# Kernel tuning notes

Measured on AMD Instinct MI355X. Metric: run time of the kernel, lower is better.

Reference implementation:

```python
import jax, jax.numpy as jnp
import numpy as np

BN_EPS = 1e-5
W_BITS = 2
A_BITS = 2


def _quantize_k(x, k):
    # uniform quantization of x in [0,1] to k bits, straight-through estimator
    n = float(2 ** k - 1)
    q = jnp.round(x * n) / n
    return x + jax.lax.stop_gradient(q - x)


def _quant_weight(w, k):
    # DoReFa-style weight quantization to [-1, 1]
    t = jnp.tanh(w)
    t = t / (2.0 * jnp.max(jnp.abs(t))) + 0.5
    return 2.0 * _quantize_k(t, k) - 1.0


def _quant_act(x, k):
    # DoReFa-style activation quantization: clamp to [0,1], quantize
    return _quantize_k(jnp.clip(x, 0.0, 1.0), k)


def _conv3x3(x, w, stride=1):
    # x: [N,C,H,W], w: [O,I,3,3], padding=1
    return jax.lax.conv_general_dilated(
        x, w, window_strides=(stride, stride), padding=((1, 1), (1, 1)),
        dimension_numbers=('NCHW', 'OIHW', 'NCHW'))


def _bn(x, gamma, beta, mean, var):
    inv = gamma / jnp.sqrt(var + BN_EPS)           # [C]
    return x * inv[None, :, None, None] + (beta - mean * inv)[None, :, None, None]


def setup_inputs() -> dict:
    key = jax.random.key(0)
    ks = jax.random.split(key, 8)
    N, C, H, W = 64, 256, 28, 28
    x = jax.random.normal(ks[0], (N, C, H, W), dtype=jnp.float32)
    w1 = jax.random.normal(ks[1], (C, C, 3, 3), dtype=jnp.float32) * 0.05
    w2 = jax.random.normal(ks[2], (C, C, 3, 3), dtype=jnp.float32) * 0.05
    g1 = jnp.ones((C,), jnp.float32)
    b1 = jnp.zeros((C,), jnp.float32)
    m1 = jax.random.normal(ks[3], (C,), dtype=jnp.float32) * 0.1
    v1 = jax.random.uniform(ks[4], (C,), dtype=jnp.float32) + 0.5
    g2 = jnp.ones((C,), jnp.float32)
    b2 = jnp.zeros((C,), jnp.float32)
    m2 = jax.random.normal(ks[5], (C,), dtype=jnp.float32) * 0.1
    v2 = jax.random.uniform(ks[6], (C,), dtype=jnp.float32) + 0.5
    return {'x': x, 'w1': w1, 'g1': g1, 'b1': b1, 'm1': m1, 'v1': v1,
            'w2': w2, 'g2': g2, 'b2': b2, 'm2': m2, 'v2': v2}


def reference(x, w1, g1, b1, m1, v1, w2, g2, b2, m2, v2):
    residual = x
    # conv1 (2-bit quantized weights & activations) -> bn1 -> relu
    out = _conv3x3(_quant_act(x, A_BITS), _quant_weight(w1, W_BITS), stride=1)
    out = jax.nn.relu(_bn(out, g1, b1, m1, v1))
    # conv2 (2-bit quantized) -> bn2
    out = _conv3x3(_quant_act(out, A_BITS), _quant_weight(w2, W_BITS), stride=1)
    out = _bn(out, g2, b2, m2, v2)
    # residual add + relu
    return jax.nn.relu(out + residual)
```

## Files before the change

kernel.cpp:

```cpp
#include <hip/hip_runtime.h>


#define ABUF 14745600
using i32x4 = __attribute__((ext_vector_type(4))) int;

__device__ __forceinline__ void gload16(const void* g, void* l) {
  typedef const __attribute__((address_space(1))) unsigned int* gp_t;
  typedef __attribute__((address_space(3))) unsigned int* lp_t;
  __builtin_amdgcn_global_load_lds((gp_t)g, (lp_t)l, 16, 0, 0);
}

__global__ void maxabs_k(const float* __restrict__ w1, const float* __restrict__ w2,
                         float* __restrict__ partial,
                         const float* g1, const float* b1, const float* m1, const float* v1,
                         const float* g2, const float* b2, const float* m2, const float* v2,
                         float* s1, float* t1, float* s2, float* t2) {
  int t = threadIdx.x, bx = blockIdx.x, ten = blockIdx.y;
  if (ten == 0 && bx == 0) {
    float i1 = g1[t] / sqrtf(v1[t] + 1e-5f);
    s1[t] = i1 * (1.f / 9.f);
    t1[t] = b1[t] - m1[t] * i1;
    float i2 = g2[t] / sqrtf(v2[t] + 1e-5f);
    s2[t] = i2 * (1.f / 9.f);
    t2[t] = b2[t] - m2[t] * i2;
  }
  const float4* v = (const float4*)(ten ? w2 : w1);
  float loc = 0.f;
  for (int i = bx * 256 + t; i < 147456; i += 16384) {
    float4 f = v[i];
    loc = fmaxf(loc, fmaxf(fmaxf(fabsf(f.x), fabsf(f.y)), fmaxf(fabsf(f.z), fabsf(f.w))));
  }
  #pragma unroll
  for (int off = 32; off; off >>= 1) loc = fmaxf(loc, __shfl_xor(loc, off));
  __shared__ float red[4];
  if ((t & 63) == 0) red[t >> 6] = loc;
  __syncthreads();
  if (t == 0)
    partial[ten * 64 + bx] = fmaxf(fmaxf(red[0], red[1]), fmaxf(red[2], red[3]));
}

__global__ void wquant_k(const float* __restrict__ w1, const float* __restrict__ w2,
                         const float* __restrict__ partial,
                         signed char* __restrict__ wq1, signed char* __restrict__ wq2) {
  const float* w = blockIdx.y ? w2 : w1;
  signed char* o = blockIdx.y ? wq2 : wq1;
  float pm = partial[blockIdx.y * 64 + (threadIdx.x & 63)];
  #pragma unroll
  for (int off = 32; off; off >>= 1) pm = fmaxf(pm, __shfl_xor(pm, off));
  float mt = tanhf(pm);
  int idx = blockIdx.x * 256 + threadIdx.x;
  int oo = idx / 2304, rr = idx % 2304, t9 = rr >> 8, ci = rr & 255;
  float t = tanhf(w[oo * 2304 + ci * 9 + t9]) / (2.f * mt) + 0.5f;
  int q = (int)rintf(t * 3.f);
  o[idx] = (signed char)(2 * q - 3);
}

__device__ __forceinline__ int border_pix(int bp) {
  int hh, ww;
  if (bp < 30)      { hh = 0;       ww = bp; }
  else if (bp < 60) { hh = 29;      ww = bp - 30; }
  else if (bp < 88) { hh = bp - 59; ww = 0; }
  else              { hh = bp - 87; ww = 29; }
  return hh * 30 + ww;
}

__global__ void aquant_k(const float* __restrict__ x, unsigned char* __restrict__ a1,
                         unsigned char* __restrict__ a2) {
  __shared__ unsigned au[784 * 17];
  const int t = threadIdx.x;
  const int n = blockIdx.x >> 2, cq = blockIdx.x & 3;
  const int c4 = t >> 4, q = t & 15;

  #pragma unroll
  for (int m = 0; m < 2; ++m) {
    int s2 = t + m * 256;
    if (s2 < 464) {
      int bp = s2 >> 2, quad = s2 & 3;
      size_t off = ((size_t)n * 900 + border_pix(bp)) * 256 + cq * 64 + quad * 16;
      uint4 z = {0, 0, 0, 0};
      *(uint4*)(a1 + off) = z;
      *(uint4*)(a2 + off) = z;
    }
  }

  const float* xb = x + (size_t)n * 200704 + (cq * 64 + c4 * 4) * 784;
  #pragma unroll
  for (int k = 0; k < 13; ++k) {
    int hw4 = q + k * 16;
    if (hw4 < 196) {
      unsigned b[4][4];
      #pragma unroll
      for (int i = 0; i < 4; ++i) {
        float4 f = *(const float4*)(xb + i * 784 + hw4 * 4);
        b[i][0] = (unsigned)(int)rintf(3.f * fminf(fmaxf(f.x, 0.f), 1.f));
        b[i][1] = (unsigned)(int)rintf(3.f * fminf(fmaxf(f.y, 0.f), 1.f));
        b[i][2] = (unsigned)(int)rintf(3.f * fminf(fmaxf(f.z, 0.f), 1.f));
        b[i][3] = (unsigned)(int)rintf(3.f * fminf(fmaxf(f.w, 0.f), 1.f));
      }
      #pragma unroll
      for (int j = 0; j < 4; ++j)
        au[(hw4 * 4 + j) * 17 + c4] = b[0][j] | (b[1][j] << 8) | (b[2][j] << 16) | (b[3][j] << 24);
    }
  }
  __syncthreads();
  #pragma unroll
  for (int m = 0; m < 13; ++m) {
    int s = t + m * 256;
    if (s < 3136) {
      int pix = s >> 2, quad = s & 3;
      uint4 v;
      v.x = au[pix * 17 + quad * 4 + 0];
      v.y = au[pix * 17 + quad * 4 + 1];
      v.z = au[pix * 17 + quad * 4 + 2];
      v.w = au[pix * 17 + quad * 4 + 3];
      int hh = pix / 28, ww = pix - hh * 28;
      *(uint4*)(a1 + (((n * 30 + hh + 1) * 30) + ww + 1) * 256 + cq * 64 + quad * 16) = v;
    }
  }
}

#define PH_MID() do { __builtin_amdgcn_s_barrier(); \
  asm volatile("s_waitcnt lgkmcnt(0)" ::: "memory"); \
  __builtin_amdgcn_sched_barrier(0); \
  __builtin_amdgcn_s_setprio(1); } while (0)
#define PH_END() do { __builtin_amdgcn_s_setprio(0); \
  __builtin_amdgcn_s_barrier(); } while (0)
#define PH_ENDV(N) do { __builtin_amdgcn_s_setprio(0); \
  asm volatile("s_waitcnt vmcnt(" #N ")" ::: "memory"); \
  __builtin_amdgcn_sched_barrier(0); \
  __builtin_amdgcn_s_barrier(); } while (0)

template <int MODE>
__global__ __launch_bounds__(512, 2) void conv_gemm(
    const unsigned char* __restrict__ act, const signed char* __restrict__ wq,
    const float* __restrict__ sC, const float* __restrict__ tC,
    const float* __restrict__ xres, unsigned char* __restrict__ actout,
    float* __restrict__ fout) {
  extern __shared__ __align__(16) char lds[];
  const int tid = threadIdx.x, wv = tid >> 6, lane = tid & 63;
  const int bswz = blockIdx.x & 7, bloc = blockIdx.x >> 3;
  const int wg = (bswz < 4 ? bswz * 25 : 100 + (bswz - 4) * 24) + bloc;
  const int pixBase = wg * 256;
  const int wvm = wv >> 2, wvn = wv & 3;
  constexpr int RAoff = (MODE == 0) ? 0 : 32768;
  constexpr int RBoff = 32768 - RAoff;

  int pixB[2][2], wB[2][2];
  {
    int s = (lane & 7) ^ ((lane >> 3) & 7);
    #pragma unroll
    for (int h = 0; h < 2; ++h)
      #pragma unroll
      for (int c = 0; c < 2; ++c) {
        int r = h * 128 + c * 64 + wv * 8 + (lane >> 3);
        int p = pixBase + r;
        int n = p / 784, rem = p % 784, hh = rem / 28, ww = rem % 28;
        pixB[h][c] = (((n * 30 + hh) * 30 + ww) << 8) + (s << 4);
        wB[h][c] = r * 2304 + (s << 4);
      }
  }
  auto tof = [](int kt) {
    int tap = kt >> 1;
    return ((tap / 3) * 30 + (tap % 3)) * 256 + ((kt & 1) << 7);
  };
  auto stagePix = [&](int h, int kt) {
    const int base = (kt & 1) * 65536 + h * 16384 + wv * 1024;
    const int toff = tof(kt);
    gload16(act + pixB[h][0] + toff, &lds[base]);
    gload16(act + pixB[h][1] + toff, &lds[base + 8192]);
  };
  auto stageW = [&](int h, int kt) {
    const int base = (kt & 1) * 65536 + 32768 + h * 16384 + wv * 1024;
    gload16(wq + wB[h][0] + kt * 128, &lds[base]);
    gload16(wq + wB[h][1] + kt * 128, &lds[base + 8192]);
  };
  auto stageA = [&](int h, int kt) { if (MODE == 0) stagePix(h, kt); else stageW(h, kt); };
  auto stageB = [&](int h, int kt) { if (MODE == 0) stageW(h, kt); else stagePix(h, kt); };

  i32x4 acc[8][4];
  #pragma unroll
  for (int i = 0; i < 8; ++i)
    #pragma unroll
    for (int j = 0; j < 4; ++j) acc[i][j] = (i32x4){0, 0, 0, 0};
  i32x4 pa[4][2], pb0[2][2], pb1[2][2];

  auto rdA = [&](int buf, int mh) {
    #pragma unroll
    for (int f = 0; f < 4; ++f) {
      int r = wvm * 128 + mh * 64 + f * 16 + (lane & 15);
      int rb = buf * 65536 + RAoff + r * 128;
      #pragma unroll
      for (int kc = 0; kc < 2; ++kc) {
        int sl = kc * 4 + (lane >> 4);
        pa[f][kc] = *(const i32x4*)&lds[rb + ((sl ^ (r & 7)) << 4)];
      }
    }
  };
  auto rdB = [&](int buf, int nh, i32x4 (*pb)[2]) {
    #pragma unroll
    for (int g = 0; g < 2; ++g) {
      int r = wvn * 64 + nh * 32 + g * 16 + (lane & 15);
      int rb = buf * 65536 + RBoff + r * 128;
      #pragma unroll
      for (int kc = 0; kc < 2; ++kc) {
        int sl = kc * 4 + (lane >> 4);
        pb[g][kc] = *(const i32x4*)&lds[rb + ((sl ^ (r & 7)) << 4)];
      }
    }
  };
  auto quad = [&](int mh, int nh, i32x4 (*pb)[2]) {
    #pragma unroll
    for (int kc = 0; kc < 2; ++kc)
      #pragma unroll
      for (int f = 0; f < 4; ++f)
        #pragma unroll
        for (int g = 0; g < 2; ++g)
          acc[mh * 4 + f][nh * 2 + g] = __builtin_amdgcn_mfma_i32_16x16x64_i8(
              pa[f][kc], pb[g][kc], acc[mh * 4 + f][nh * 2 + g], 0, 0, 0);
  };

  stageB(0, 0); stageA(0, 0); stageB(1, 0); stageA(1, 0);
  stageB(0, 1); stageA(0, 1); stageB(1, 1);
  asm volatile("s_waitcnt vmcnt(6)" ::: "memory");
  __builtin_amdgcn_sched_barrier(0);
  __builtin_amdgcn_s_barrier();

  for (int it = 0; it < 9; ++it) {
    const int ktY = 2 * it + 1, ktX2 = 2 * it + 2, ktY2 = 2 * it + 3;
    const bool st = (it < 8);
    rdA(0, 0); rdB(0, 0, pb0);
    stageA(1, ktY);
    PH_MID(); quad(0, 0, pb0); PH_END();
    rdB(0, 1, pb1);
    PH_MID(); quad(0, 1, pb1); PH_END();
    rdA(0, 1);
    if (st) stageB(0, ktX2);
    PH_MID(); quad(1, 0, pb0); PH_END();
    if (st) { stageA(0, ktX2); stageB(1, ktX2); }
    PH_MID(); quad(1, 1, pb1);
    if (st) { PH_ENDV(6); } else { PH_ENDV(0); }
    rdA(1, 0); rdB(1, 0, pb0);
    if (st) stageA(1, ktX2);
    PH_MID(); quad(0, 0, pb0); PH_END();
    rdB(1, 1, pb1);
    PH_MID(); quad(0, 1, pb1); PH_END();
    rdA(1, 1);
    if (st) stageB(0, ktY2);
    PH_MID(); quad(1, 0, pb0); PH_END();
    if (st) { stageA(0, ktY2); stageB(1, ktY2); }
    PH_MID(); quad(1, 1, pb1);
    PH_ENDV(6);
  }

  if (MODE == 0) {
    float sj[4], tj[4];
    #pragma unroll
    for (int j = 0; j < 4; ++j) {
      int c = wvn * 64 + j * 16 + (lane & 15);
      sj[j] = sC[c]; tj[j] = tC[c];
    }
    __syncthreads();
    #pragma unroll
    for (int i = 0; i < 8; ++i) {
      int lp0 = wvm * 128 + i * 16 + ((lane >> 4) << 2);
      #pragma unroll
      for (int j = 0; j < 4; ++j) {
        int lch = wvn * 64 + j * 16 + (lane & 15);
        #pragma unroll
        for (int r = 0; r < 4; ++r) {
          float y = (float)acc[i][j][r] * sj[j] + tj[j];
          y = fminf(fmaxf(y, 0.f), 1.f);
          int lp = lp0 + r;
          lds[lp * 256 + (lch ^ ((lp & 7) << 4))] = (char)(int)rintf(y * 3.f);
        }
      }
    }
    __syncthreads();
    int rr = tid >> 1, hf = tid & 1;
    int p = pixBase + rr;
    int n = p / 784, rem = p % 784, hh = rem / 28, ww = rem % 28;
    unsigned char* dst = actout + (((n * 30 + hh + 1) * 30 + (ww + 1)) << 8) + hf * 128;
    #pragma unroll
    for (int k = 0; k < 8; ++k) {
      uint4 v = *(const uint4*)&lds[rr * 256 + ((hf * 128 + k * 16) ^ ((rr & 7) << 4))];
      *(uint4*)(dst + k * 16) = v;
    }
  } else {
    float* ldsf = (float*)lds;
    const int half = tid >> 8, row = (tid >> 4) & 15, seg = tid & 15;
    #pragma unroll
    for (int s = 0; s < 8; ++s) {
      float* dst = ldsf + (s & 1) * 8448 + wvm * 4224;
      #pragma unroll
      for (int j = 0; j < 4; ++j)
        #pragma unroll
        for (int r = 0; r < 4; ++r)
          dst[(((lane >> 4) << 2) + r) * 264 + wvn * 64 + j * 16 + (lane & 15)] =
              (float)acc[s][j][r];
      __syncthreads();
      int c = half * 128 + s * 16 + row;
      float sc = sC[c], tc = tC[c];
      const float* src = ldsf + (s & 1) * 8448 + half * 4224 + row * 264 + seg * 16;
      const float* xrc = xres + (size_t)c * 784;
      float* foc = fout + (size_t)c * 784;
      #pragma unroll
      for (int f = 0; f < 4; ++f) {
        int p = pixBase + seg * 16 + f * 4;
        int n = p / 784, rem = p - n * 784;
        float4 v = *(const float4*)(src + f * 4);
        float4 xr = *(const float4*)(xrc + n * 200704 + rem);
        float4 y;
        y.x = fmaxf(v.x * sc + tc + xr.x, 0.f);
        y.y = fmaxf(v.y * sc + tc + xr.y, 0.f);
        y.z = fmaxf(v.z * sc + tc + xr.z, 0.f);
        y.w = fmaxf(v.w * sc + tc + xr.w, 0.f);
        *(float4*)(foc + n * 200704 + rem) = y;
      }
    }
  }
}

extern "C" void kernel_launch(void* const* d_in, const int* in_sizes, int n_in,
                              void* d_out, int out_size, void* d_ws, size_t ws_size,
                              hipStream_t stream) {
  const float* x  = (const float*)d_in[0];
  const float* w1 = (const float*)d_in[1];
  const float* g1 = (const float*)d_in[2];
  const float* b1 = (const float*)d_in[3];
  const float* m1 = (const float*)d_in[4];
  const float* v1 = (const float*)d_in[5];
  const float* w2 = (const float*)d_in[6];
  const float* g2 = (const float*)d_in[7];
  const float* b2 = (const float*)d_in[8];
  const float* m2 = (const float*)d_in[9];
  const float* v2 = (const float*)d_in[10];

  char* ws = (char*)d_ws;
  float* partial = (float*)ws;
  float* s1 = (float*)(ws + 1024);
  float* t1 = (float*)(ws + 2048);
  float* s2 = (float*)(ws + 3072);
  float* t2 = (float*)(ws + 4096);
  unsigned char* a1 = (unsigned char*)(ws + 8192);
  unsigned char* a2 = a1 + ABUF;
  signed char* wq1 = (signed char*)(a2 + ABUF);
  signed char* wq2 = wq1 + 589824;

  void (*k0)(const unsigned char*, const signed char*, const float*, const float*,
             const float*, unsigned char*, float*) = conv_gemm<0>;
  void (*k1)(const unsigned char*, const signed char*, const float*, const float*,
             const float*, unsigned char*, float*) = conv_gemm<1>;
  hipFuncSetAttribute((const void*)k0, hipFuncAttributeMaxDynamicSharedMemorySize, 131072);
  hipFuncSetAttribute((const void*)k1, hipFuncAttributeMaxDynamicSharedMemorySize, 131072);

  maxabs_k<<<dim3(64, 2), 256, 0, stream>>>(w1, w2, partial,
                                            g1, b1, m1, v1, g2, b2, m2, v2,
                                            s1, t1, s2, t2);
  wquant_k<<<dim3(2304, 2), 256, 0, stream>>>(w1, w2, partial, wq1, wq2);
  aquant_k<<<256, 256, 0, stream>>>(x, a1, a2);
  conv_gemm<0><<<196, 512, 131072, stream>>>(a1, wq1, s1, t1, nullptr, a2, nullptr);
  conv_gemm<1><<<196, 512, 131072, stream>>>(a2, wq2, s2, t2, x, nullptr, (float*)d_out);
}
```

Before: 221.1 us.

## Merge prep kernels, coalesce weight quantization, and store conv2 epilogue from registers

The max-abs reduction and BN folding are merged into the activation-quantize kernel as extra blocks, which removes one launch. Weight quantization now works per output channel: it stages tanh values in LDS so global reads are coalesced, and it launches 256x2 blocks instead of 2304x2. The conv2 epilogue drops the LDS round-trip and its barriers. It transposes accumulators across lanes with DPP moves and writes float4 results straight to global memory. The residual reads and output writes may coalesce less well than the old row-organized LDS path.

Result: faster. 204.6 us (-7.5%).

```diff
diff --git a/kernel.cpp b/kernel.cpp
--- a/kernel.cpp
+++ b/kernel.cpp
@@ -8,51 +8,6 @@
   typedef const __attribute__((address_space(1))) unsigned int* gp_t;
   typedef __attribute__((address_space(3))) unsigned int* lp_t;
   __builtin_amdgcn_global_load_lds((gp_t)g, (lp_t)l, 16, 0, 0);
-}
-
-__global__ void maxabs_k(const float* __restrict__ w1, const float* __restrict__ w2,
-                         float* __restrict__ partial,
-                         const float* g1, const float* b1, const float* m1, const float* v1,
-                         const float* g2, const float* b2, const float* m2, const float* v2,
-                         float* s1, float* t1, float* s2, float* t2) {
-  int t = threadIdx.x, bx = blockIdx.x, ten = blockIdx.y;
-  if (ten == 0 && bx == 0) {
-    float i1 = g1[t] / sqrtf(v1[t] + 1e-5f);
-    s1[t] = i1 * (1.f / 9.f);
-    t1[t] = b1[t] - m1[t] * i1;
-    float i2 = g2[t] / sqrtf(v2[t] + 1e-5f);
-    s2[t] = i2 * (1.f / 9.f);
-    t2[t] = b2[t] - m2[t] * i2;
-  }
-  const float4* v = (const float4*)(ten ? w2 : w1);
-  float loc = 0.f;
-  for (int i = bx * 256 + t; i < 147456; i += 16384) {
-    float4 f = v[i];
-    loc = fmaxf(loc, fmaxf(fmaxf(fabsf(f.x), fabsf(f.y)), fmaxf(fabsf(f.z), fabsf(f.w))));
-  }
-  #pragma unroll
-  for (int off = 32; off; off >>= 1) loc = fmaxf(loc, __shfl_xor(loc, off));
-  __shared__ float red[4];
-  if ((t & 63) == 0) red[t >> 6] = loc;
-  __syncthreads();
-  if (t == 0)
-    partial[ten * 64 + bx] = fmaxf(fmaxf(red[0], red[1]), fmaxf(red[2], red[3]));
-}
-
-__global__ void wquant_k(const float* __restrict__ w1, const float* __restrict__ w2,
-                         const float* __restrict__ partial,
-                         signed char* __restrict__ wq1, signed char* __restrict__ wq2) {
-  const float* w = blockIdx.y ? w2 : w1;
-  signed char* o = blockIdx.y ? wq2 : wq1;
-  float pm = partial[blockIdx.y * 64 + (threadIdx.x & 63)];
-  #pragma unroll
-  for (int off = 32; off; off >>= 1) pm = fmaxf(pm, __shfl_xor(pm, off));
-  float mt = tanhf(pm);
-  int idx = blockIdx.x * 256 + threadIdx.x;
-  int oo = idx / 2304, rr = idx % 2304, t9 = rr >> 8, ci = rr & 255;
-  float t = tanhf(w[oo * 2304 + ci * 9 + t9]) / (2.f * mt) + 0.5f;
-  int q = (int)rintf(t * 3.f);
-  o[idx] = (signed char)(2 * q - 3);
 }
 
 __device__ __forceinline__ int border_pix(int bp) {
@@ -64,18 +19,49 @@
   return hh * 30 + ww;
 }
 
-__global__ void aquant_k(const float* __restrict__ x, unsigned char* __restrict__ a1,
-                         unsigned char* __restrict__ a2) {
+__global__ void pre_k(const float* __restrict__ x, unsigned char* __restrict__ a1,
+                      unsigned char* __restrict__ a2,
+                      const float* __restrict__ w1, const float* __restrict__ w2,
+                      float* __restrict__ partial,
+                      const float* g1, const float* b1, const float* m1, const float* v1,
+                      const float* g2, const float* b2, const float* m2, const float* v2,
+                      float* s1, float* t1, float* s2, float* t2) {
+  const int t = threadIdx.x;
+  if (blockIdx.x >= 256) {
+    int bx = blockIdx.x - 256;
+    int ten = bx >> 6, bxl = bx & 63;
+    if (ten == 0 && bxl == 0) {
+      float i1 = g1[t] / sqrtf(v1[t] + 1e-5f);
+      s1[t] = i1 * (1.f / 9.f);
+      t1[t] = b1[t] - m1[t] * i1;
+      float i2 = g2[t] / sqrtf(v2[t] + 1e-5f);
+      s2[t] = i2 * (1.f / 9.f);
+      t2[t] = b2[t] - m2[t] * i2;
+    }
+    const float4* v = (const float4*)(ten ? w2 : w1);
+    float loc = 0.f;
+    for (int i = bxl * 256 + t; i < 147456; i += 16384) {
+      float4 f = v[i];
+      loc = fmaxf(loc, fmaxf(fmaxf(fabsf(f.x), fabsf(f.y)), fmaxf(fabsf(f.z), fabsf(f.w))));
+    }
+    #pragma unroll
+    for (int off = 32; off; off >>= 1) loc = fmaxf(loc, __shfl_xor(loc, off));
+    __shared__ float red[4];
+    if ((t & 63) == 0) red[t >> 6] = loc;
+    __syncthreads();
+    if (t == 0)
+      partial[ten * 64 + bxl] = fmaxf(fmaxf(red[0], red[1]), fmaxf(red[2], red[3]));
+    return;
+  }
   __shared__ unsigned au[784 * 17];
-  const int t = threadIdx.x;
   const int n = blockIdx.x >> 2, cq = blockIdx.x & 3;
   const int c4 = t >> 4, q = t & 15;
 
   #pragma unroll
   for (int m = 0; m < 2; ++m) {
-    int s2 = t + m * 256;
-    if (s2 < 464) {
-      int bp = s2 >> 2, quad = s2 & 3;
+    int s2i = t + m * 256;
+    if (s2i < 464) {
+      int bp = s2i >> 2, quad = s2i & 3;
       size_t off = ((size_t)n * 900 + border_pix(bp)) * 256 + cq * 64 + quad * 16;
       uint4 z = {0, 0, 0, 0};
       *(uint4*)(a1 + off) = z;
@@ -116,6 +102,30 @@
       int hh = pix / 28, ww = pix - hh * 28;
       *(uint4*)(a1 + (((n * 30 + hh + 1) * 30) + ww + 1) * 256 + cq * 64 + quad * 16) = v;
     }
+  }
+}
+
+__global__ void wquant_k(const float* __restrict__ w1, const float* __restrict__ w2,
+                         const float* __restrict__ partial,
+                         signed char* __restrict__ wq1, signed char* __restrict__ wq2) {
+  const int oo = blockIdx.x, ten = blockIdx.y;
+  const float* w = ten ? w2 : w1;
+  signed char* o = ten ? wq2 : wq1;
+  __shared__ float wl[2304];
+  const int t = threadIdx.x;
+  float pm = partial[ten * 64 + (t & 63)];
+  #pragma unroll
+  for (int off = 32; off; off >>= 1) pm = fmaxf(pm, __shfl_xor(pm, off));
+  const float inv = 1.f / (2.f * tanhf(pm));
+  #pragma unroll
+  for (int k = 0; k < 9; ++k) wl[k * 256 + t] = tanhf(w[oo * 2304 + k * 256 + t]);
+  __syncthreads();
+  #pragma unroll
+  for (int k = 0; k < 9; ++k) {
+    int j = k * 256 + t, t9 = j >> 8, ci = j & 255;
+    float tt = wl[ci * 9 + t9] * inv + 0.5f;
+    int q = (int)rintf(tt * 3.f);
+    o[oo * 2304 + j] = (signed char)(2 * q - 3);
   }
 }
 
@@ -286,35 +296,41 @@
       *(uint4*)(dst + k * 16) = v;
     }
   } else {
-    float* ldsf = (float*)lds;
-    const int half = tid >> 8, row = (tid >> 4) & 15, seg = tid & 15;
-    #pragma unroll
-    for (int s = 0; s < 8; ++s) {
-      float* dst = ldsf + (s & 1) * 8448 + wvm * 4224;
-      #pragma unroll
-      for (int j = 0; j < 4; ++j)
-        #pragma unroll
-        for (int r = 0; r < 4; ++r)
-          dst[(((lane >> 4) << 2) + r) * 264 + wvn * 64 + j * 16 + (lane & 15)] =
-              (float)acc[s][j][r];
-      __syncthreads();
-      int c = half * 128 + s * 16 + row;
+    #pragma unroll
+    for (int i = 0; i < 8; ++i) {
+      int c = wvm * 128 + i * 16 + ((lane >> 4) << 2) + (lane & 3);
       float sc = sC[c], tc = tC[c];
-      const float* src = ldsf + (s & 1) * 8448 + half * 4224 + row * 264 + seg * 16;
-      const float* xrc = xres + (size_t)c * 784;
-      float* foc = fout + (size_t)c * 784;
-      #pragma unroll
-      for (int f = 0; f < 4; ++f) {
-        int p = pixBase + seg * 16 + f * 4;
-        int n = p / 784, rem = p - n * 784;
-        float4 v = *(const float4*)(src + f * 4);
-        float4 xr = *(const float4*)(xrc + n * 200704 + rem);
+      #pragma unroll
+      for (int j = 0; j < 4; ++j) {
+        int a0 = acc[i][j][0], a1 = acc[i][j][1], a2 = acc[i][j][2], a3 = acc[i][j][3];
+        int t0 = __builtin_amdgcn_mov_dpp(a0, 0xB1, 0xF, 0xF, true);
+        int t1 = __builtin_amdgcn_mov_dpp(a1, 0xB1, 0xF, 0xF, true);
+        int t2 = __builtin_amdgcn_mov_dpp(a2, 0xB1, 0xF, 0xF, true);
+        int t3 = __builtin_amdgcn_mov_dpp(a3, 0xB1, 0xF, 0xF, true);
+        const bool o1 = (lane & 1) != 0;
+        int v0 = o1 ? t1 : a0;
+        int v1 = o1 ? a1 : t0;
+        int v2 = o1 ? t3 : a2;
+        int v3 = o1 ? a3 : t2;
+        int u0 = __builtin_amdgcn_mov_dpp(v2, 0x4E, 0xF, 0xF, true);
+        int u1 = __builtin_amdgcn_mov_dpp(v3, 0x4E, 0xF, 0xF, true);
+        int u2 = __builtin_amdgcn_mov_dpp(v0, 0x4E, 0xF, 0xF, true);
+        int u3 = __builtin_amdgcn_mov_dpp(v1, 0x4E, 0xF, 0xF, true);
+        const bool o2 = (lane & 2) != 0;
+        int z0 = o2 ? u0 : v0;
+        int z1 = o2 ? u1 : v1;
+        int z2 = o2 ? v2 : u2;
+        int z3 = o2 ? v3 : u3;
+        int P = pixBase + wvn * 64 + j * 16 + (lane & 12);
+        int n = P / 784, rem = P - n * 784;
+        size_t addr = (size_t)n * 200704 + (size_t)c * 784 + rem;
+        float4 xr = *(const float4*)(xres + addr);
         float4 y;
-        y.x = fmaxf(v.x * sc + tc + xr.x, 0.f);
-        y.y = fmaxf(v.y * sc + tc + xr.y, 0.f);
-        y.z = fmaxf(v.z * sc + tc + xr.z, 0.f);
-        y.w = fmaxf(v.w * sc + tc + xr.w, 0.f);
-        *(float4*)(foc + n * 200704 + rem) = y;
+        y.x = fmaxf((float)z0 * sc + tc + xr.x, 0.f);
+        y.y = fmaxf((float)z1 * sc + tc + xr.y, 0.f);
+        y.z = fmaxf((float)z2 * sc + tc + xr.z, 0.f);
+        y.w = fmaxf((float)z3 * sc + tc + xr.w, 0.f);
+        *(float4*)(fout + addr) = y;
       }
     }
   }
@@ -353,11 +369,9 @@
   hipFuncSetAttribute((const void*)k0, hipFuncAttributeMaxDynamicSharedMemorySize, 131072);
   hipFuncSetAttribute((const void*)k1, hipFuncAttributeMaxDynamicSharedMemorySize, 131072);
 
-  maxabs_k<<<dim3(64, 2), 256, 0, stream>>>(w1, w2, partial,
-                                            g1, b1, m1, v1, g2, b2, m2, v2,
-                                            s1, t1, s2, t2);
-  wquant_k<<<dim3(2304, 2), 256, 0, stream>>>(w1, w2, partial, wq1, wq2);
-  aquant_k<<<256, 256, 0, stream>>>(x, a1, a2);
+  pre_k<<<384, 256, 0, stream>>>(x, a1, a2, w1, w2, partial,
+                                 g1, b1, m1, v1, g2, b2, m2, v2, s1, t1, s2, t2);
+  wquant_k<<<dim3(256, 2), 256, 0, stream>>>(w1, w2, partial, wq1, wq2);
   conv_gemm<0><<<196, 512, 131072, stream>>>(a1, wq1, s1, t1, nullptr, a2, nullptr);
   conv_gemm<1><<<196, 512, 131072, stream>>>(a2, wq2, s2, t2, x, nullptr, (float*)d_out);
 }
```
